# Optimization experiments

Measured on AMD Instinct MI355X. Metric: run time of the kernel, lower is better.

Reference implementation:

```python
import jax, jax.numpy as jnp
import numpy as np

H = 1024
F = 132

def _lstm_cell(x, h, c, Wih, Whh, bih, bhh):
    # PyTorch LSTMCell: gates ordered i, f, g, o
    gates = x @ Wih.T + bih + h @ Whh.T + bhh  # [B, 4H]
    i, f, g, o = jnp.split(gates, 4, axis=-1)
    i = jax.nn.sigmoid(i)
    f = jax.nn.sigmoid(f)
    g = jnp.tanh(g)
    o = jax.nn.sigmoid(o)
    c_new = f * c + i * g
    h_new = o * jnp.tanh(c_new)
    return h_new, c_new


def setup_inputs() -> dict:
    key = jax.random.key(0)
    ks = jax.random.split(key, 16)
    s = 0.02
    return {
        "initial_seq": jax.random.normal(ks[0], (32, 64, F), dtype=jnp.float32),
        "generate_frames_number": 128,
        "W_ih1": jax.random.normal(ks[1], (4 * H, F), dtype=jnp.float32) * s,
        "W_hh1": jax.random.normal(ks[2], (4 * H, H), dtype=jnp.float32) * s,
        "b_ih1": jax.random.normal(ks[3], (4 * H,), dtype=jnp.float32) * s,
        "b_hh1": jax.random.normal(ks[4], (4 * H,), dtype=jnp.float32) * s,
        "W_ih2": jax.random.normal(ks[5], (4 * H, H), dtype=jnp.float32) * s,
        "W_hh2": jax.random.normal(ks[6], (4 * H, H), dtype=jnp.float32) * s,
        "b_ih2": jax.random.normal(ks[7], (4 * H,), dtype=jnp.float32) * s,
        "b_hh2": jax.random.normal(ks[8], (4 * H,), dtype=jnp.float32) * s,
        "W_ih3": jax.random.normal(ks[9], (4 * H, H), dtype=jnp.float32) * s,
        "W_hh3": jax.random.normal(ks[10], (4 * H, H), dtype=jnp.float32) * s,
        "b_ih3": jax.random.normal(ks[11], (4 * H,), dtype=jnp.float32) * s,
        "b_hh3": jax.random.normal(ks[12], (4 * H,), dtype=jnp.float32) * s,
        "W_dec": jax.random.normal(ks[13], (F, H), dtype=jnp.float32) * s,
        "b_dec": jax.random.normal(ks[14], (F,), dtype=jnp.float32) * s,
    }


def reference(initial_seq, generate_frames_number,
              W_ih1, W_hh1, b_ih1, b_hh1,
              W_ih2, W_hh2, b_ih2, b_hh2,
              W_ih3, W_hh3, b_ih3, b_hh3,
              W_dec, b_dec):
    B = initial_seq.shape[0]
    dt = initial_seq.dtype
    zeros = jnp.zeros((B, H), dtype=dt)
    state0 = (zeros, zeros, zeros, zeros, zeros, zeros)  # h0,h1,h2,c0,c1,c2

    def step(state, in_frame):
        h0, h1, h2, c0, c1, c2 = state
        h0, c0 = _lstm_cell(in_frame, h0, c0, W_ih1, W_hh1, b_ih1, b_hh1)
        h1, c1 = _lstm_cell(h0, h1, c1, W_ih2, W_hh2, b_ih2, b_hh2)
        h2, c2 = _lstm_cell(h1, h2, c2, W_ih3, W_hh3, b_ih3, b_hh3)
        out_frame = h2 @ W_dec.T + b_dec  # [B, F]
        return (h0, h1, h2, c0, c1, c2), out_frame

    # Priming pass over the conditioning sequence (outputs discarded except last)
    def prime_step(carry, in_frame):
        state, _ = carry
        state, out = step(state, in_frame)
        return (state, out), None

    init_frame = jnp.zeros((B, F), dtype=dt)
    xs = jnp.swapaxes(initial_seq, 0, 1)  # [T, B, F]
    (state, cur_frame), _ = jax.lax.scan(prime_step, (state0, init_frame), xs)

    def gen_step(carry, _):
        state, frame = carry
        state, out = step(state, frame)
        return (state, out), out

    _, outs = jax.lax.scan(gen_step, (state, cur_frame), None,
                           length=generate_frames_number)  # [N, B, F]
    return jnp.swapaxes(outs, 0, 1)  # [B, N, F]
```

## Files before the change

kernel.cpp:

```cpp
#include <hip/hip_runtime.h>
#include <stdint.h>

typedef unsigned short u16;
typedef unsigned long long u64;
typedef __attribute__((ext_vector_type(8))) short short8;
typedef __attribute__((ext_vector_type(4))) float f32x4;

#define SZ_BIGW    (4096ull*1024ull*2ull)
#define OFF_WHH1   (0ull)
#define OFF_WIH2   (OFF_WHH1 + SZ_BIGW)
#define OFF_WHH2   (OFF_WIH2 + SZ_BIGW)
#define OFF_WIH3   (OFF_WHH2 + SZ_BIGW)
#define OFF_WHH3   (OFF_WIH3 + SZ_BIGW)
#define OFF_MCOMB  (OFF_WHH3 + SZ_BIGW)
#define OFF_WIH1   (OFF_MCOMB + SZ_BIGW)
#define SZ_WIH1    (4096ull*160ull*2ull)
#define OFF_WDECF  (OFF_WIH1 + SZ_WIH1)
#define SZ_WDECF   (160ull*1024ull*2ull)
#define OFF_WDECB  (OFF_WDECF + SZ_WDECF)
#define SZ_WDECB   (1024ull*160ull*2ull)
#define OFF_XPRIM  (OFF_WDECB + SZ_WDECB)
#define SZ_XPRIM   (64ull*5120ull*2ull)
#define OFF_H2HIST (OFF_XPRIM + SZ_XPRIM)
#define SZ_HSLOT   (32768ull*2ull)
#define SZ_H2HIST  (129ull*SZ_HSLOT)
#define OFF_H0R    (OFF_H2HIST + SZ_H2HIST)
#define SZ_HR      (192ull*SZ_HSLOT)
#define OFF_H1R    (OFF_H0R + SZ_HR)
#define OFF_H2R    (OFF_H1R + SZ_HR)
#define SZ_H2R     (64ull*SZ_HSLOT)
#define OFF_ZEROH  (OFF_H2R + SZ_H2R)
#define OFF_FLAGS  (OFF_ZEROH + SZ_HSLOT)
#define SZ_FLAGS   (4096ull)
#define OFF_BS1    (OFF_FLAGS + SZ_FLAGS)
#define OFF_BS1G   (OFF_BS1 + 16384ull)
#define OFF_BS2    (OFF_BS1G + 16384ull)
#define OFF_BS3    (OFF_BS2 + 16384ull)
#define BLOB_SIZE  (OFF_BS3 + 16384ull)

__device__ unsigned char g_blob[BLOB_SIZE];

#define ZERO_BYTES (SZ_HSLOT + SZ_FLAGS)

__device__ __forceinline__ u16 f2bf(float f) {
  unsigned u = __float_as_uint(f);
  u += 0x7fffu + ((u >> 16) & 1u);
  return (u16)(u >> 16);
}
__device__ __forceinline__ float sigm(float x) { return 1.f / (1.f + __expf(-x)); }
__device__ __forceinline__ float tanh_(float x) {
  x = fminf(fmaxf(x, -40.f), 40.f);
  float e = __expf(2.f * x);
  return (e - 1.f) / (e + 1.f);
}

__global__ __launch_bounds__(256) void k_zero(uint4* p, int n) {
  int i = blockIdx.x * 256 + threadIdx.x;
  for (; i < n; i += gridDim.x * 256) p[i] = make_uint4(0u, 0u, 0u, 0u);
}

__global__ __launch_bounds__(256) void k_swizzle(const float* __restrict__ src, u16* __restrict__ dst,
                                                 int J, int Jsrc, int Kpad, int Ksrc, int srcld,
                                                 int transposed, int perm) {
  int total = J * Kpad;
  int nkc = Kpad >> 3;
  for (int o = blockIdx.x * 256 + threadIdx.x; o < total; o += gridDim.x * 256) {
    int chunk = o >> 7, within = o & 127;
    int nt = chunk / nkc, kc = chunk - nt * nkc;
    int jr = within >> 3, ke = within & 7;
    int j = perm ? ((jr >> 2) * 1024 + nt * 4 + (jr & 3)) : (nt * 16 + jr);
    int k = kc * 8 + ke;
    float v = 0.f;
    if (j < Jsrc && k < Ksrc)
      v = transposed ? src[(size_t)k * srcld + j] : src[(size_t)j * srcld + k];
    dst[o] = f2bf(v);
  }
}

__global__ __launch_bounds__(256) void k_xprim(const float* __restrict__ iseq, u16* __restrict__ dst) {
  int o = blockIdx.x * 256 + threadIdx.x;
  if (o >= 64 * 5120) return;
  int t = o / 5120, rem = o - t * 5120;
  int kc = rem >> 8, b = (rem >> 3) & 31, ke = rem & 7;
  int k = kc * 8 + ke;
  float v = (k < 132) ? iseq[(size_t)b * (64 * 132) + t * 132 + k] : 0.f;
  dst[o] = f2bf(v);
}

__global__ __launch_bounds__(256) void k_bias(const float* bih1, const float* bhh1,
                                              const float* bih2, const float* bhh2,
                                              const float* bih3, const float* bhh3,
                                              const float* __restrict__ Wih1, const float* __restrict__ bdec,
                                              float* bs1, float* bs1g, float* bs2, float* bs3) {
  int j = blockIdx.x * 256 + threadIdx.x;
  if (j >= 4096) return;
  float s1 = bih1[j] + bhh1[j];
  float bc = 0.f;
  const float* wr = Wih1 + (size_t)j * 132;
  for (int f = 0; f < 132; ++f) bc += wr[f] * bdec[f];
  bs1[j] = s1;
  bs1g[j] = s1 + bc;
  bs2[j] = bih2[j] + bhh2[j];
  bs3[j] = bih3[j] + bhh3[j];
}

__global__ __launch_bounds__(256) void k_mcomb(const u16* __restrict__ A, const u16* __restrict__ Bm,
                                               u16* __restrict__ dst) {
  int blk = blockIdx.x;
  int mt = blk & 255, jg = blk >> 8;
  int w = threadIdx.x >> 6, l = threadIdx.x & 63, q = l >> 4, r = l & 15;
  int nt = jg * 4 + w;
  f32x4 acc = {};
  for (int ks = 0; ks < 5; ++ks) {
    short8 a = *(const short8*)(A + ((size_t)mt * 20 + ks * 4 + q) * 128 + r * 8);
    short8 b = *(const short8*)(Bm + ((size_t)nt * 20 + ks * 4 + q) * 128 + r * 8);
    acc = __builtin_amdgcn_mfma_f32_16x16x32_bf16(a, b, acc, 0, 0, 0);
  }
  int kout = nt * 16 + r;
#pragma unroll
  for (int i = 0; i < 4; ++i) {
    int jrow = q * 4 + i;
    dst[(((size_t)mt * 128 + (kout >> 3)) << 7) + jrow * 8 + (kout & 7)] = f2bf(acc[i]);
  }
}


__device__ __forceinline__ void wait_all(unsigned* F, unsigned tgt) {
  if (threadIdx.x < 256) {
    while (__hip_atomic_load(F + threadIdx.x, __ATOMIC_RELAXED, __HIP_MEMORY_SCOPE_AGENT) < tgt)
      __builtin_amdgcn_s_sleep(1);
  }
  __syncthreads();
}

#define MFMA(a, b, c) __builtin_amdgcn_mfma_f32_16x16x32_bf16((a), (b), (c), 0, 0, 0)

__device__ __forceinline__ void seg_mm(f32x4& a0, f32x4& a1,
                                       const u16* __restrict__ x, const short8 (&wt)[4],
                                       int w, int q, int r) {
#pragma unroll
  for (int i = 0; i < 4; ++i) {
    const u16* xp = x + (w + 8 * i) * 1024 + q * 256 + r * 8;
    short8 t0 = *(const short8*)(xp);
    short8 t1 = *(const short8*)(xp + 128);
    a0 = MFMA(t0, wt[i], a0);
    a1 = MFMA(t1, wt[i], a1);
  }
}

template<int LBASE>
__device__ __forceinline__ void gen_phase(
    f32x4& acc0, f32x4& acc1,
    const u16* __restrict__ xa, const short8 (&wA)[4],
    unsigned* waitF, unsigned wtgt,
    const float* __restrict__ bsum, float& creg, u16* __restrict__ hout,
    unsigned* arrF, unsigned aval,
    float (*red)[2][256], u64* hstage, int nt)
{
  int tid = threadIdx.x;
  int w = tid >> 6, l = tid & 63, q = l >> 4, r = l & 15;

  wait_all(waitF, wtgt);

#pragma unroll
  for (int i = 0; i < 4; ++i) {
    const u16* xp = xa + (w + 8 * i) * 1024 + q * 256 + r * 8;
    short8 a0 = *(const short8*)(xp);
    short8 a1 = *(const short8*)(xp + 128);
    acc0 = MFMA(a0, wA[i], acc0);
    acc1 = MFMA(a1, wA[i], acc1);
  }

  *(f32x4*)&red[w][0][l * 4] = acc0;
  *(f32x4*)&red[w][1][l * 4] = acc1;
  __syncthreads();

  if (tid >= LBASE && tid < LBASE + 128) {
    int idx = tid - LBASE;
    int b = idx >> 2, hl = idx & 3, mt = b >> 4, row = b & 15;
    int j0 = nt * 4 + hl;
    float g4[4];
#pragma unroll
    for (int g = 0; g < 4; ++g) {
      int col = g * 4 + hl;
      int lidx = ((row >> 2) * 16 + col) * 4 + (row & 3);
      float s = bsum[g * 1024 + j0];
#pragma unroll
      for (int ww = 0; ww < 8; ++ww) s += red[ww][mt][lidx];
      g4[g] = s;
    }
    float iv = sigm(g4[0]), fv = sigm(g4[1]), gv = tanh_(g4[2]), ov = sigm(g4[3]);
    float cn = fv * creg + iv * gv;
    creg = cn;
    ((u16*)hstage)[LBASE + idx] = f2bf(ov * tanh_(cn));
  }
  __syncthreads();

  if (tid < 64) {
    if (tid < 32) {
      u64 v = hstage[(LBASE >> 2) + tid];
      u64* dp = (u64*)(hout + ((size_t)(nt >> 1) * 256 + tid * 8 + (nt & 1) * 4));
      __hip_atomic_store(dp, v, __ATOMIC_RELAXED, __HIP_MEMORY_SCOPE_AGENT);
    }
    asm volatile("s_waitcnt vmcnt(0)" ::: "memory");
    if (tid == 0)
      __hip_atomic_store(arrF + nt, aval, __ATOMIC_RELAXED, __HIP_MEMORY_SCOPE_AGENT);
  }
}

__global__ __launch_bounds__(512, 1) void k_rnn(unsigned char* blob) {
  __shared__ float red3[3][8][2][256];
  __shared__ u64 hstage[96];
  const u16* XPRIM = (const u16*)(blob + OFF_XPRIM);
  const u16* tWIH1 = (const u16*)(blob + OFF_WIH1);
  const u16* tMCOMB = (const u16*)(blob + OFF_MCOMB);
  const u16* tWHH1 = (const u16*)(blob + OFF_WHH1);
  const u16* tWIH2 = (const u16*)(blob + OFF_WIH2);
  const u16* tWHH2 = (const u16*)(blob + OFF_WHH2);
  const u16* tWIH3 = (const u16*)(blob + OFF_WIH3);
  const u16* tWHH3 = (const u16*)(blob + OFF_WHH3);
  const float* BS1 = (const float*)(blob + OFF_BS1);
  const float* BS1G = (const float*)(blob + OFF_BS1G);
  const float* BS2 = (const float*)(blob + OFF_BS2);
  const float* BS3 = (const float*)(blob + OFF_BS3);
  u16* H0R = (u16*)(blob + OFF_H0R);
  u16* H1R = (u16*)(blob + OFF_H1R);
  u16* H2R = (u16*)(blob + OFF_H2R);
  u16* H2HIST = (u16*)(blob + OFF_H2HIST);
  const u16* ZEROH = (const u16*)(blob + OFF_ZEROH);
  unsigned* FLAGS = (unsigned*)(blob + OFF_FLAGS);
  unsigned *FP = FLAGS, *F1 = FLAGS + 256, *F2 = FLAGS + 512, *F3 = FLAGS + 768;

  int nt = blockIdx.x;
  int tid = threadIdx.x;
  int w = tid >> 6, l = tid & 63, q = l >> 4, r = l & 15;
  int layer = tid >> 7, idx = tid & 127;
  const float* BSP = (layer == 0) ? BS1 : (layer == 1) ? BS2 : BS3;
  float creg = 0.f;

  short8 rWhh1[4], rWih2[4], rWhh2[4], rWih3[4], rWhh3[4];
#pragma unroll
  for (int i = 0; i < 4; ++i) {
    size_t off = (size_t)nt * 16384 + (size_t)(w + 8 * i) * 512 + (size_t)l * 8;
    rWhh1[i] = *(const short8*)(tWHH1 + off);
    rWih2[i] = *(const short8*)(tWIH2 + off);
    rWhh2[i] = *(const short8*)(tWHH2 + off);
    rWih3[i] = *(const short8*)(tWIH3 + off);
    rWhh3[i] = *(const short8*)(tWHH3 + off);
  }
  short8 rWih1 = {};
  if (w < 5)
    rWih1 = *(const short8*)(tWIH1 + (size_t)nt * 2560 + (size_t)w * 512 + (size_t)l * 8);

  for (int b = 0; b < 66; ++b) {
    f32x4 a10 = {}, a11 = {}, a20 = {}, a21 = {}, a30 = {}, a31 = {};

    if (b < 64 && w < 5) {
      const u16* xp = XPRIM + b * 5120 + w * 1024 + q * 256 + r * 8;
      short8 x0 = *(const short8*)(xp);
      short8 x1 = *(const short8*)(xp + 128);
      a10 = MFMA(x0, rWih1, a10);
      a11 = MFMA(x1, rWih1, a11);
    }

    wait_all(FP, (unsigned)b);

    if (b <= 64) {
      const u16* h0p = (b == 0) ? ZEROH : H0R + (size_t)(b - 1) * 32768;
#pragma unroll
      for (int i = 0; i < 4; ++i) {
        const u16* xp = h0p + (w + 8 * i) * 1024 + q * 256 + r * 8;
        short8 x0_ = *(const short8*)(xp);
        short8 x1_ = *(const short8*)(xp + 128);
        if (b <= 63) { a10 = MFMA(x0_, rWhh1[i], a10); a11 = MFMA(x1_, rWhh1[i], a11); }
        if (b >= 1)  { a20 = MFMA(x0_, rWih2[i], a20); a21 = MFMA(x1_, rWih2[i], a21); }
      }
    }
    if (b >= 1) {
      const u16* h1p = (b == 1) ? ZEROH : H1R + (size_t)(b - 2) * 32768;
#pragma unroll
      for (int i = 0; i < 4; ++i) {
        const u16* xp = h1p + (w + 8 * i) * 1024 + q * 256 + r * 8;
        short8 x0_ = *(const short8*)(xp);
        short8 x1_ = *(const short8*)(xp + 128);
        if (b <= 64) { a20 = MFMA(x0_, rWhh2[i], a20); a21 = MFMA(x1_, rWhh2[i], a21); }
        if (b >= 2)  { a30 = MFMA(x0_, rWih3[i], a30); a31 = MFMA(x1_, rWih3[i], a31); }
      }
    }
    if (b >= 2) {
      const u16* h2p = (b == 2) ? ZEROH : H2R + (size_t)(b - 3) * 32768;
#pragma unroll
      for (int i = 0; i < 4; ++i) {
        const u16* xp = h2p + (w + 8 * i) * 1024 + q * 256 + r * 8;
        short8 x0_ = *(const short8*)(xp);
        short8 x1_ = *(const short8*)(xp + 128);
        a30 = MFMA(x0_, rWhh3[i], a30);
        a31 = MFMA(x1_, rWhh3[i], a31);
      }
    }

    *(f32x4*)&red3[0][w][0][l * 4] = a10;  *(f32x4*)&red3[0][w][1][l * 4] = a11;
    *(f32x4*)&red3[1][w][0][l * 4] = a20;  *(f32x4*)&red3[1][w][1][l * 4] = a21;
    *(f32x4*)&red3[2][w][0][l * 4] = a30;  *(f32x4*)&red3[2][w][1][l * 4] = a31;
    __syncthreads();

    int tb = b - layer;
    if (tid < 384 && tb >= 0 && tb <= 63) {
      int bb = idx >> 2, hl = idx & 3, mt = bb >> 4, row = bb & 15;
      int j0 = nt * 4 + hl;
      float g4[4];
#pragma unroll
      for (int g = 0; g < 4; ++g) {
        int col = g * 4 + hl;
        int lidx = ((row >> 2) * 16 + col) * 4 + (row & 3);
        float s = BSP[g * 1024 + j0];
#pragma unroll
        for (int ww = 0; ww < 8; ++ww) s += red3[layer][ww][mt][lidx];
        g4[g] = s;
      }
      float iv = sigm(g4[0]), fv = sigm(g4[1]), gv = tanh_(g4[2]), ov = sigm(g4[3]);
      float cn = fv * creg + iv * gv;
      creg = cn;
      ((u16*)hstage)[tid] = f2bf(ov * tanh_(cn));
    }
    __syncthreads();

    if (tid < 64) {
      if (tid < 32) {
        size_t doff = (size_t)(nt >> 1) * 256 + (size_t)tid * 8 + (size_t)(nt & 1) * 4;
        if (b <= 63)
          __hip_atomic_store((u64*)(H0R + (size_t)b * 32768 + doff), hstage[tid],
                             __ATOMIC_RELAXED, __HIP_MEMORY_SCOPE_AGENT);
        if (b >= 1 && b <= 64)
          __hip_atomic_store((u64*)(H1R + (size_t)(b - 1) * 32768 + doff), hstage[32 + tid],
                             __ATOMIC_RELAXED, __HIP_MEMORY_SCOPE_AGENT);
        if (b >= 2) {
          u16* dst = (b < 65) ? (H2R + (size_t)(b - 2) * 32768) : H2HIST;
          __hip_atomic_store((u64*)(dst + doff), hstage[64 + tid],
                             __ATOMIC_RELAXED, __HIP_MEMORY_SCOPE_AGENT);
        }
      }
      asm volatile("s_waitcnt vmcnt(0)" ::: "memory");
      if (tid == 0)
        __hip_atomic_store(FP + nt, (unsigned)(b + 1), __ATOMIC_RELAXED, __HIP_MEMORY_SCOPE_AGENT);
    }
  }

  short8 rMcomb[4];
#pragma unroll
  for (int i = 0; i < 4; ++i)
    rMcomb[i] = *(const short8*)(tMCOMB + (size_t)nt * 16384 + (size_t)(w + 8 * i) * 512 + (size_t)l * 8);

  f32x4 c10, c11, c20, c21, c30, c31;

  c10 = {}; c11 = {};
  seg_mm(c10, c11, H0R + (size_t)63 * 32768, rWhh1, w, q, r);

  for (int t = 64; t < 192; ++t) {
    c20 = {}; c21 = {};
    seg_mm(c20, c21, H1R + (size_t)(t - 1) * 32768, rWhh2, w, q, r);

    gen_phase<0>(c10, c11, H2HIST + (size_t)(t - 64) * 32768, rMcomb,
                 (t == 64) ? FP : F3, (t == 64) ? 66u : (unsigned)(t - 64),
                 BS1G, creg, H0R + (size_t)t * 32768,
                 F1, (unsigned)(t - 63), red3[0], hstage, nt);

    c30 = {}; c31 = {};
    seg_mm(c30, c31, H2HIST + (size_t)(t - 64) * 32768, rWhh3, w, q, r);

    gen_phase<128>(c20, c21, H0R + (size_t)t * 32768, rWih2,
                   F1, (unsigned)(t - 63),
                   BS2, creg, H1R + (size_t)t * 32768,
                   F2, (unsigned)(t - 63), red3[0], hstage, nt);

    c10 = {}; c11 = {};
    if (t < 191)
      seg_mm(c10, c11, H0R + (size_t)t * 32768, rWhh1, w, q, r);

    gen_phase<256>(c30, c31, H1R + (size_t)t * 32768, rWih3,
                   F2, (unsigned)(t - 63),
                   BS3, creg, H2HIST + (size_t)(t - 63) * 32768,
                   F3, (unsigned)(t - 63), red3[0], hstage, nt);
  }
}

__global__ __launch_bounds__(256) void k_dec(const u16* __restrict__ h2hist, const u16* __restrict__ Wd,
                                             const float* __restrict__ bdec, float* __restrict__ out) {
  int blk = blockIdx.x;
  int s = blk / 10, nt = blk - s * 10;
  const u16* x = h2hist + (size_t)(s + 1) * 32768;
  int w = threadIdx.x >> 6, l = threadIdx.x & 63, q = l >> 4, r = l & 15;
  f32x4 acc[2] = {};
  for (int ks = w; ks < 32; ks += 4) {
    const u16* xp = x + ks * 1024 + q * 256 + r * 8;
    short8 a0 = *(const short8*)(xp);
    short8 a1 = *(const short8*)(xp + 128);
    short8 bf = *(const short8*)(Wd + (((size_t)nt * 128 + ks * 4) << 7) + l * 8);
    acc[0] = __builtin_amdgcn_mfma_f32_16x16x32_bf16(a0, bf, acc[0], 0, 0, 0);
    acc[1] = __builtin_amdgcn_mfma_f32_16x16x32_bf16(a1, bf, acc[1], 0, 0, 0);
  }
  __shared__ float red[4][2][256];
#pragma unroll
  for (int mt = 0; mt < 2; ++mt)
#pragma unroll
    for (int i = 0; i < 4; ++i) red[w][mt][l * 4 + i] = acc[mt][i];
  __syncthreads();
  for (int pp = threadIdx.x; pp < 512; pp += 256) {
    int b = pp >> 4, fs = pp & 15;
    int mt = b >> 4, row = b & 15;
    int lidx = ((row >> 2) * 16 + fs) * 4 + (row & 3);
    int f = nt * 16 + fs;
    if (f < 132) {
      float v = red[0][mt][lidx] + red[1][mt][lidx] + red[2][mt][lidx] + red[3][mt][lidx] + bdec[f];
      out[(size_t)b * (128 * 132) + s * 132 + f] = v;
    }
  }
}

extern "C" void kernel_launch(void* const* d_in, const int* in_sizes, int n_in,
                              void* d_out, int out_size, void* d_ws, size_t ws_size,
                              hipStream_t stream) {
  unsigned char* blob = nullptr;
  hipGetSymbolAddress((void**)&blob, HIP_SYMBOL(g_blob));

  const float* iseq = (const float*)d_in[0];
  const float* Wih1 = (const float*)d_in[2];
  const float* Whh1 = (const float*)d_in[3];
  const float* bih1 = (const float*)d_in[4];
  const float* bhh1 = (const float*)d_in[5];
  const float* Wih2 = (const float*)d_in[6];
  const float* Whh2 = (const float*)d_in[7];
  const float* bih2 = (const float*)d_in[8];
  const float* bhh2 = (const float*)d_in[9];
  const float* Wih3 = (const float*)d_in[10];
  const float* Whh3 = (const float*)d_in[11];
  const float* bih3 = (const float*)d_in[12];
  const float* bhh3 = (const float*)d_in[13];
  const float* Wdec = (const float*)d_in[14];
  const float* bdec = (const float*)d_in[15];

  u16* tWHH1 = (u16*)(blob + OFF_WHH1);
  u16* tWIH2 = (u16*)(blob + OFF_WIH2);
  u16* tWHH2 = (u16*)(blob + OFF_WHH2);
  u16* tWIH3 = (u16*)(blob + OFF_WIH3);
  u16* tWHH3 = (u16*)(blob + OFF_WHH3);
  u16* tMCOMB = (u16*)(blob + OFF_MCOMB);
  u16* tWIH1 = (u16*)(blob + OFF_WIH1);
  u16* tWDECF = (u16*)(blob + OFF_WDECF);
  u16* tWDECB = (u16*)(blob + OFF_WDECB);
  u16* XPRIM = (u16*)(blob + OFF_XPRIM);
  u16* H2HIST = (u16*)(blob + OFF_H2HIST);
  float* BS1 = (float*)(blob + OFF_BS1);
  float* BS1G = (float*)(blob + OFF_BS1G);
  float* BS2 = (float*)(blob + OFF_BS2);
  float* BS3 = (float*)(blob + OFF_BS3);

  k_zero<<<68, 256, 0, stream>>>((uint4*)(blob + OFF_ZEROH), (int)(ZERO_BYTES / 16));
  k_swizzle<<<2048, 256, 0, stream>>>(Whh1, tWHH1, 4096, 4096, 1024, 1024, 1024, 0, 1);
  k_swizzle<<<2048, 256, 0, stream>>>(Wih2, tWIH2, 4096, 4096, 1024, 1024, 1024, 0, 1);
  k_swizzle<<<2048, 256, 0, stream>>>(Whh2, tWHH2, 4096, 4096, 1024, 1024, 1024, 0, 1);
  k_swizzle<<<2048, 256, 0, stream>>>(Wih3, tWIH3, 4096, 4096, 1024, 1024, 1024, 0, 1);
  k_swizzle<<<2048, 256, 0, stream>>>(Whh3, tWHH3, 4096, 4096, 1024, 1024, 1024, 0, 1);
  k_swizzle<<<2048, 256, 0, stream>>>(Wih1, tWIH1, 4096, 4096, 160, 132, 132, 0, 1);
  k_swizzle<<<512, 256, 0, stream>>>(Wdec, tWDECF, 160, 132, 1024, 1024, 1024, 0, 0);
  k_swizzle<<<512, 256, 0, stream>>>(Wdec, tWDECB, 1024, 1024, 160, 132, 1024, 1, 0);
  k_xprim<<<1280, 256, 0, stream>>>(iseq, XPRIM);
  k_bias<<<16, 256, 0, stream>>>(bih1, bhh1, bih2, bhh2, bih3, bhh3, Wih1, bdec, BS1, BS1G, BS2, BS3);
  k_mcomb<<<4096, 256, 0, stream>>>(tWIH1, tWDECB, tMCOMB);

  {
    void* args[] = { (void*)&blob };
    hipError_t ce = hipLaunchCooperativeKernel((void*)k_rnn, dim3(256), dim3(512), args, 0, stream);
    if (ce != hipSuccess) {
      k_rnn<<<dim3(256), dim3(512), 0, stream>>>(blob);
    }
  }

  k_dec<<<1280, 256, 0, stream>>>(H2HIST, tWDECF, bdec, (float*)d_out);
}
```

Measured before the change: 2.253 ms.

## Replace per-block flag arrays with per-epoch atomic arrival counters

Grid-wide synchronization moves from 256 threads each polling one of 256 per-block flags to a single thread polling one counter per epoch. Each block signals arrival with an atomic add on that epoch's counter, and epochs are numbered sequentially across the priming and generation phases. This is meant to cut polling traffic and wait latency at each grid barrier. The trade-off is that 256 blocks now contend for atomics on the same address, and the counter region must be zeroed before each launch.

Measured after the change: 3.121 ms. 38.5% more time.

```diff
diff --git a/kernel.cpp b/kernel.cpp
--- a/kernel.cpp
+++ b/kernel.cpp
@@ -125,9 +125,9 @@
 }
 
 
-__device__ __forceinline__ void wait_all(unsigned* F, unsigned tgt) {
-  if (threadIdx.x < 256) {
-    while (__hip_atomic_load(F + threadIdx.x, __ATOMIC_RELAXED, __HIP_MEMORY_SCOPE_AGENT) < tgt)
+__device__ __forceinline__ void wait_epoch(unsigned* C, unsigned e) {
+  if (threadIdx.x == 0) {
+    while (__hip_atomic_load(C + e, __ATOMIC_RELAXED, __HIP_MEMORY_SCOPE_AGENT) < 256u)
       __builtin_amdgcn_s_sleep(1);
   }
   __syncthreads();
@@ -152,15 +152,15 @@
 __device__ __forceinline__ void gen_phase(
     f32x4& acc0, f32x4& acc1,
     const u16* __restrict__ xa, const short8 (&wA)[4],
-    unsigned* waitF, unsigned wtgt,
+    unsigned* CNT, unsigned waitE,
     const float* __restrict__ bsum, float& creg, u16* __restrict__ hout,
-    unsigned* arrF, unsigned aval,
+    unsigned relE,
     float (*red)[2][256], u64* hstage, int nt)
 {
   int tid = threadIdx.x;
   int w = tid >> 6, l = tid & 63, q = l >> 4, r = l & 15;
 
-  wait_all(waitF, wtgt);
+  wait_epoch(CNT, waitE);
 
 #pragma unroll
   for (int i = 0; i < 4; ++i) {
@@ -204,7 +204,7 @@
     }
     asm volatile("s_waitcnt vmcnt(0)" ::: "memory");
     if (tid == 0)
-      __hip_atomic_store(arrF + nt, aval, __ATOMIC_RELAXED, __HIP_MEMORY_SCOPE_AGENT);
+      __hip_atomic_fetch_add(CNT + relE, 1u, __ATOMIC_RELAXED, __HIP_MEMORY_SCOPE_AGENT);
   }
 }
 
@@ -228,8 +228,7 @@
   u16* H2R = (u16*)(blob + OFF_H2R);
   u16* H2HIST = (u16*)(blob + OFF_H2HIST);
   const u16* ZEROH = (const u16*)(blob + OFF_ZEROH);
-  unsigned* FLAGS = (unsigned*)(blob + OFF_FLAGS);
-  unsigned *FP = FLAGS, *F1 = FLAGS + 256, *F2 = FLAGS + 512, *F3 = FLAGS + 768;
+  unsigned* CNT = (unsigned*)(blob + OFF_FLAGS);
 
   int nt = blockIdx.x;
   int tid = threadIdx.x;
@@ -263,7 +262,8 @@
       a11 = MFMA(x1, rWih1, a11);
     }
 
-    wait_all(FP, (unsigned)b);
+    if (b > 0) wait_epoch(CNT, (unsigned)b);
+    else __syncthreads();
 
     if (b <= 64) {
       const u16* h0p = (b == 0) ? ZEROH : H0R + (size_t)(b - 1) * 32768;
@@ -342,7 +342,7 @@
       }
       asm volatile("s_waitcnt vmcnt(0)" ::: "memory");
       if (tid == 0)
-        __hip_atomic_store(FP + nt, (unsigned)(b + 1), __ATOMIC_RELAXED, __HIP_MEMORY_SCOPE_AGENT);
+        __hip_atomic_fetch_add(CNT + (unsigned)(b + 1), 1u, __ATOMIC_RELAXED, __HIP_MEMORY_SCOPE_AGENT);
     }
   }
 
@@ -361,26 +361,26 @@
     seg_mm(c20, c21, H1R + (size_t)(t - 1) * 32768, rWhh2, w, q, r);
 
     gen_phase<0>(c10, c11, H2HIST + (size_t)(t - 64) * 32768, rMcomb,
-                 (t == 64) ? FP : F3, (t == 64) ? 66u : (unsigned)(t - 64),
+                 CNT, (t == 64) ? 66u : (unsigned)(3 * t - 126),
                  BS1G, creg, H0R + (size_t)t * 32768,
-                 F1, (unsigned)(t - 63), red3[0], hstage, nt);
+                 (unsigned)(3 * t - 125), red3[0], hstage, nt);
 
     c30 = {}; c31 = {};
     seg_mm(c30, c31, H2HIST + (size_t)(t - 64) * 32768, rWhh3, w, q, r);
 
     gen_phase<128>(c20, c21, H0R + (size_t)t * 32768, rWih2,
-                   F1, (unsigned)(t - 63),
+                   CNT, (unsigned)(3 * t - 125),
                    BS2, creg, H1R + (size_t)t * 32768,
-                   F2, (unsigned)(t - 63), red3[0], hstage, nt);
+                   (unsigned)(3 * t - 124), red3[0], hstage, nt);
 
     c10 = {}; c11 = {};
     if (t < 191)
       seg_mm(c10, c11, H0R + (size_t)t * 32768, rWhh1, w, q, r);
 
     gen_phase<256>(c30, c31, H1R + (size_t)t * 32768, rWih3,
-                   F2, (unsigned)(t - 63),
+                   CNT, (unsigned)(3 * t - 124),
                    BS3, creg, H2HIST + (size_t)(t - 63) * 32768,
-                   F3, (unsigned)(t - 63), red3[0], hstage, nt);
+                   (unsigned)(3 * t - 123), red3[0], hstage, nt);
   }
 }
 
```
